# Kernel tuning notes

Hardware: AMD Instinct MI355X
Metric: run time of the kernel (lower is better)

The kernel has to match this reference:

```python
import jax, jax.numpy as jnp
import numpy as np
from jax import lax

_SOBEL_X = jnp.array([[-1., 0., 1.], [-2., 0., 2.], [-1., 0., 1.]], dtype=jnp.float32)
_SOBEL_Y = jnp.array([[1., 2., 1.], [0., 0., 0.], [-1., -2., -1.]], dtype=jnp.float32)


def rgb2ycrcb(x):
    # x: [B,3,H,W] -> [B,3,H,W] (Y, Cr, Cb)
    R, G, B = x[:, 0], x[:, 1], x[:, 2]
    Y = 0.299 * R + 0.587 * G + 0.114 * B
    Cr = (R - Y) * 0.713 + 0.5
    Cb = (B - Y) * 0.564 + 0.5
    return jnp.stack([Y, Cr, Cb], axis=1)


def depthwise_sobel(x):
    # x: [B,3,H,W]; per-channel 3x3 cross-correlation with SAME padding (matches F.conv2d pad=1)
    C = x.shape[1]
    wx = jnp.broadcast_to(_SOBEL_X[None, None], (C, 1, 3, 3))
    wy = jnp.broadcast_to(_SOBEL_Y[None, None], (C, 1, 3, 3))
    dn = ('NCHW', 'OIHW', 'NCHW')
    gx = lax.conv_general_dilated(x, wx, (1, 1), 'SAME', feature_group_count=C, dimension_numbers=dn)
    gy = lax.conv_general_dilated(x, wy, (1, 1), 'SAME', feature_group_count=C, dimension_numbers=dn)
    return gx, gy


def adjust_gamma(img, gamma, gain=1.0):
    # torchvision float path: clamp(gain * img**gamma, 0, 1)
    return jnp.clip(gain * img ** gamma, 0.0, 1.0)


def adjust_contrast(img, factor):
    # torchvision: blend with per-image mean of grayscale, then clamp
    gray = 0.2989 * img[:, 0:1] + 0.587 * img[:, 1:2] + 0.114 * img[:, 2:3]
    mean = jnp.mean(gray, axis=(1, 2, 3), keepdims=True)
    return jnp.clip(factor * img + (1.0 - factor) * mean, 0.0, 1.0)


def l1(a, b):
    return jnp.mean(jnp.abs(a - b))


def fusion_loss(input_vis, input_ir, output, Mask):
    Fuse = output * Mask
    ycc_fuse = rgb2ycrcb(Fuse)
    Cr_F, Cb_F = ycc_fuse[:, 1:2], ycc_fuse[:, 2:3]

    R_vis = adjust_gamma(input_vis, 0.5, 1.0)
    ycc_vis = rgb2ycrcb(R_vis)
    Cr_V, Cb_V = ycc_vis[:, 1:2], ycc_vis[:, 2:3]

    R_ir = adjust_contrast(input_ir, 1.8)

    fgx, fgy = depthwise_sobel(Fuse)
    vgx, vgy = depthwise_sobel(R_vis)
    igx, igy = depthwise_sobel(R_ir)

    joint_gx = jnp.maximum(vgx, igx)
    joint_gy = jnp.maximum(vgy, igy)
    joint_int = jnp.maximum(R_vis, R_ir)

    con_loss = l1(Fuse, joint_int)
    grad_loss = 0.5 * l1(fgx, joint_gx) + 0.5 * l1(fgy, joint_gy)
    color_loss = l1(Cb_F, Cb_V) + l1(Cr_F, Cr_V)
    return 0.5 * con_loss + 0.2 * grad_loss + 1.0 * color_loss


def setup_inputs() -> dict:
    key = jax.random.key(0)
    k1, k2, k3, k4 = jax.random.split(key, 4)
    B, C, H, W = 16, 3, 512, 512
    return {
        'input_vis': jax.random.uniform(k1, (B, C, H, W), dtype=jnp.float32),
        'input_ir': jax.random.uniform(k2, (B, C, H, W), dtype=jnp.float32),
        'output': jax.random.uniform(k3, (B, C, H, W), dtype=jnp.float32),
        'Mask': jax.random.uniform(k4, (B, C, H, W), dtype=jnp.float32),
    }


def reference(input_vis, input_ir, output, Mask):
    return fusion_loss(input_vis, input_ir, output, Mask)
```

## Files before the change

### kernel.cpp

```cpp
#include <hip/hip_runtime.h>
#include <math.h>

#define Bn 16
#define Cn 3
#define Hn 512
#define Wn 512
#define HWn (Hn*Wn)
#define CHWn (Cn*HWn)
#define Rr 4

__device__ __forceinline__ float clamp01(float x) {
    return fminf(fmaxf(x, 0.0f), 1.0f);
}

__global__ __launch_bounds__(256) void gray_mean_kernel(
        const float* __restrict__ ir, float* __restrict__ ws)
{
    const int b = blockIdx.y;
    const int tid = threadIdx.x;
    const float* base = ir + (size_t)b * CHWn;

    float sr = 0.f, sg = 0.f, sb = 0.f;
#pragma unroll
    for (int k = 0; k < 8; ++k) {
        size_t px = (size_t)blockIdx.x * 8192 + (size_t)(k * 256 + tid) * 4;
        float4 r4 = *(const float4*)(base + px);
        float4 g4 = *(const float4*)(base + HWn + px);
        float4 b4 = *(const float4*)(base + 2 * HWn + px);
        sr += (r4.x + r4.y) + (r4.z + r4.w);
        sg += (g4.x + g4.y) + (g4.z + g4.w);
        sb += (b4.x + b4.y) + (b4.z + b4.w);
    }
    float s = 0.2989f * sr + 0.587f * sg + 0.114f * sb;

#pragma unroll
    for (int off = 32; off; off >>= 1) s += __shfl_down(s, off, 64);

    __shared__ float red[4];
    if ((tid & 63) == 0) red[tid >> 6] = s;
    __syncthreads();
    if (tid == 0) atomicAdd(&ws[b], (red[0] + red[1]) + (red[2] + red[3]));
}

__global__ __launch_bounds__(256) void fusion_main_kernel(
        const float* __restrict__ vis, const float* __restrict__ ir,
        const float* __restrict__ outp, const float* __restrict__ mask,
        float* __restrict__ ws)
{
    const int tid = threadIdx.x;
    const int tx = tid & 127;
    const int sy = tid >> 7;
    const int b  = blockIdx.y;
    const int y0 = (blockIdx.x * 2 + sy) * Rr;
    const int x0 = tx * 4;

    const float mean_b = ws[b] * (1.0f / (float)HWn);
    const float moff = 0.8f * mean_b;

    const size_t bb = (size_t)b * CHWn;
    const float* pv = vis  + bb;
    const float* pi = ir   + bb;
    const float* po = outp + bb;
    const float* pm = mask + bb;

    float conA = 0.f, gxA = 0.f, gyA = 0.f;

#define DECL_SLOT(S)                                                          \
    float wf##S##_0, wf##S##_1, wf##S##_2, wf##S##_3, wf##S##_4, wf##S##_5;   \
    float wv##S##_0, wv##S##_1, wv##S##_2, wv##S##_3, wv##S##_4, wv##S##_5;   \
    float wi##S##_0, wi##S##_1, wi##S##_2, wi##S##_3, wi##S##_4, wi##S##_5;

#define LOAD_ROW(Y, S)                                                        \
    do {                                                                      \
        const int y_ = (Y);                                                   \
        if ((unsigned)y_ < (unsigned)Hn) {                                    \
            const size_t o = (size_t)y_ * Wn + x0;                            \
            float4 o4 = *(const float4*)(o_ + o);                             \
            float4 m4 = *(const float4*)(m_ + o);                             \
            float4 v4 = *(const float4*)(v_ + o);                             \
            float4 i4 = *(const float4*)(i_ + o);                             \
            float oL = 0.f, mL = 0.f, vL = 0.f, iL = 0.f;                     \
            float oR = 0.f, mR = 0.f, vR = 0.f, iR = 0.f;                     \
            if (x0 > 0)      { oL = o_[o - 1]; mL = m_[o - 1];                \
                               vL = v_[o - 1]; iL = i_[o - 1]; }              \
            if (x0 + 4 < Wn) { oR = o_[o + 4]; mR = m_[o + 4];                \
                               vR = v_[o + 4]; iR = i_[o + 4]; }              \
            wf##S##_0 = oL * mL;     wf##S##_1 = o4.x * m4.x;                 \
            wf##S##_2 = o4.y * m4.y; wf##S##_3 = o4.z * m4.z;                 \
            wf##S##_4 = o4.w * m4.w; wf##S##_5 = oR * mR;                     \
            wv##S##_0 = clamp01(sqrtf(vL));   wv##S##_1 = clamp01(sqrtf(v4.x)); \
            wv##S##_2 = clamp01(sqrtf(v4.y)); wv##S##_3 = clamp01(sqrtf(v4.z)); \
            wv##S##_4 = clamp01(sqrtf(v4.w)); wv##S##_5 = clamp01(sqrtf(vR));   \
            wi##S##_0 = clamp01(fmaf(1.8f, iL,   -moff));                     \
            wi##S##_1 = clamp01(fmaf(1.8f, i4.x, -moff));                     \
            wi##S##_2 = clamp01(fmaf(1.8f, i4.y, -moff));                     \
            wi##S##_3 = clamp01(fmaf(1.8f, i4.z, -moff));                     \
            wi##S##_4 = clamp01(fmaf(1.8f, i4.w, -moff));                     \
            wi##S##_5 = clamp01(fmaf(1.8f, iR,   -moff));                     \
        } else {                                                              \
            wf##S##_0=0.f; wf##S##_1=0.f; wf##S##_2=0.f;                      \
            wf##S##_3=0.f; wf##S##_4=0.f; wf##S##_5=0.f;                      \
            wv##S##_0=0.f; wv##S##_1=0.f; wv##S##_2=0.f;                      \
            wv##S##_3=0.f; wv##S##_4=0.f; wv##S##_5=0.f;                      \
            wi##S##_0=0.f; wi##S##_1=0.f; wi##S##_2=0.f;                      \
            wi##S##_3=0.f; wi##S##_4=0.f; wi##S##_5=0.f;                      \
        }                                                                     \
    } while (0)

#define SOBEL_J(A, B, C, J0, J1, J2)                                          \
    do {                                                                      \
        float gxf = (wf##A##_##J2 - wf##A##_##J0) + 2.f * (wf##B##_##J2 - wf##B##_##J0) + (wf##C##_##J2 - wf##C##_##J0); \
        float gyf = (wf##A##_##J0 + 2.f * wf##A##_##J1 + wf##A##_##J2) - (wf##C##_##J0 + 2.f * wf##C##_##J1 + wf##C##_##J2); \
        float gxv = (wv##A##_##J2 - wv##A##_##J0) + 2.f * (wv##B##_##J2 - wv##B##_##J0) + (wv##C##_##J2 - wv##C##_##J0); \
        float gyv = (wv##A##_##J0 + 2.f * wv##A##_##J1 + wv##A##_##J2) - (wv##C##_##J0 + 2.f * wv##C##_##J1 + wv##C##_##J2); \
        float gxi = (wi##A##_##J2 - wi##A##_##J0) + 2.f * (wi##B##_##J2 - wi##B##_##J0) + (wi##C##_##J2 - wi##C##_##J0); \
        float gyi = (wi##A##_##J0 + 2.f * wi##A##_##J1 + wi##A##_##J2) - (wi##C##_##J0 + 2.f * wi##C##_##J1 + wi##C##_##J2); \
        gxA  += fabsf(gxf - fmaxf(gxv, gxi));                                 \
        gyA  += fabsf(gyf - fmaxf(gyv, gyi));                                 \
        conA += fabsf(wf##B##_##J1 - fmaxf(wv##B##_##J1, wi##B##_##J1));      \
    } while (0)

#define STEP(A, B, C)                                                         \
    SOBEL_J(A, B, C, 0, 1, 2); SOBEL_J(A, B, C, 1, 2, 3);                     \
    SOBEL_J(A, B, C, 2, 3, 4); SOBEL_J(A, B, C, 3, 4, 5)

    for (int c = 0; c < 3; ++c) {
        const float* v_ = pv + (size_t)c * HWn;
        const float* i_ = pi + (size_t)c * HWn;
        const float* o_ = po + (size_t)c * HWn;
        const float* m_ = pm + (size_t)c * HWn;

        DECL_SLOT(0) DECL_SLOT(1) DECL_SLOT(2)

        LOAD_ROW(y0 - 1, 0);
        LOAD_ROW(y0,     1);
        LOAD_ROW(y0 + 1, 2); STEP(0, 1, 2);
        LOAD_ROW(y0 + 2, 0); STEP(1, 2, 0);
        LOAD_ROW(y0 + 3, 1); STEP(2, 0, 1);
        LOAD_ROW(y0 + 4, 2); STEP(0, 1, 2);
    }
#undef STEP
#undef SOBEL_J
#undef LOAD_ROW
#undef DECL_SLOT

    float crA = 0.f, cbA = 0.f;
    {
        for (int y = y0; y < y0 + Rr; ++y) {
            size_t o = (size_t)y * Wn + x0;
            float4 oR = *(const float4*)(po + o);
            float4 oG = *(const float4*)(po + HWn + o);
            float4 oB = *(const float4*)(po + 2 * HWn + o);
            float4 mR = *(const float4*)(pm + o);
            float4 mG = *(const float4*)(pm + HWn + o);
            float4 mB = *(const float4*)(pm + 2 * HWn + o);
            float4 vR = *(const float4*)(pv + o);
            float4 vG = *(const float4*)(pv + HWn + o);
            float4 vB = *(const float4*)(pv + 2 * HWn + o);
#define COLOR_PX(FR, FG, FB, VR, VG, VB)                                      \
            do {                                                              \
                float fr = (FR), fg = (FG), fb = (FB);                        \
                float vr = (VR), vg = (VG), vb = (VB);                        \
                float fY = 0.299f * fr + 0.587f * fg + 0.114f * fb;           \
                float vY = 0.299f * vr + 0.587f * vg + 0.114f * vb;           \
                crA += fabsf((fr - fY) * 0.713f - (vr - vY) * 0.713f);        \
                cbA += fabsf((fb - fY) * 0.564f - (vb - vY) * 0.564f);        \
            } while (0)
            COLOR_PX(oR.x * mR.x, oG.x * mG.x, oB.x * mB.x,
                     clamp01(sqrtf(vR.x)), clamp01(sqrtf(vG.x)), clamp01(sqrtf(vB.x)));
            COLOR_PX(oR.y * mR.y, oG.y * mG.y, oB.y * mB.y,
                     clamp01(sqrtf(vR.y)), clamp01(sqrtf(vG.y)), clamp01(sqrtf(vB.y)));
            COLOR_PX(oR.z * mR.z, oG.z * mG.z, oB.z * mB.z,
                     clamp01(sqrtf(vR.z)), clamp01(sqrtf(vG.z)), clamp01(sqrtf(vB.z)));
            COLOR_PX(oR.w * mR.w, oG.w * mG.w, oB.w * mB.w,
                     clamp01(sqrtf(vR.w)), clamp01(sqrtf(vG.w)), clamp01(sqrtf(vB.w)));
#undef COLOR_PX
        }
    }

    auto wred = [](float x) {
#pragma unroll
        for (int off = 32; off; off >>= 1) x += __shfl_down(x, off, 64);
        return x;
    };
    conA = wred(conA); gxA = wred(gxA); gyA = wred(gyA);
    crA  = wred(crA);  cbA = wred(cbA);

    __shared__ float red[5][4];
    const int lane = tid & 63, w = tid >> 6;
    if (lane == 0) {
        red[0][w] = conA; red[1][w] = gxA; red[2][w] = gyA;
        red[3][w] = crA;  red[4][w] = cbA;
    }
    __syncthreads();
    if (tid < 5) {
        float s = (red[tid][0] + red[tid][1]) + (red[tid][2] + red[tid][3]);
        atomicAdd(&ws[16 + tid], s);
    }
}

__global__ void finalize_kernel(const float* __restrict__ ws, float* __restrict__ out)
{
    if (threadIdx.x == 0 && blockIdx.x == 0) {
        const float invN3 = 1.0f / (float)((size_t)Bn * Cn * HWn);
        const float invN1 = 1.0f / (float)((size_t)Bn * HWn);
        float con = ws[16] * invN3;
        float gx  = ws[17] * invN3;
        float gy  = ws[18] * invN3;
        float cr  = ws[19] * invN1;
        float cb  = ws[20] * invN1;
        out[0] = 0.5f * con + 0.2f * (0.5f * gx + 0.5f * gy) + (cb + cr);
    }
}

extern "C" void kernel_launch(void* const* d_in, const int* in_sizes, int n_in,
                              void* d_out, int out_size, void* d_ws, size_t ws_size,
                              hipStream_t stream)
{
    const float* vis = (const float*)d_in[0];
    const float* ir  = (const float*)d_in[1];
    const float* out = (const float*)d_in[2];
    const float* msk = (const float*)d_in[3];
    float* ws = (float*)d_ws;

    hipMemsetAsync(ws, 0, 32 * sizeof(float), stream);

    gray_mean_kernel<<<dim3(32, Bn), 256, 0, stream>>>(ir, ws);
    fusion_main_kernel<<<dim3(Hn / (2 * Rr), Bn), 256, 0, stream>>>(vis, ir, out, msk, ws);
    finalize_kernel<<<1, 64, 0, stream>>>(ws, (float*)d_out);
}
```

Baseline: 244.6 us.

## Fuse gray-mean, main loss and finalize into one persistent kernel with grid barrier

Merges the three kernels into one 512-block launch. Each block first computes a partial IR grayscale mean, then all blocks wait at an atomic-counter grid barrier, after which each block processes two batch images' strips. The last block to finish computes the final loss, replacing the separate finalize launch. This removes two kernel launches and their gaps, but needs all 512 blocks co-resident for the spin barrier to avoid deadlock, and halves the main-phase block count (1024 to 512) while doubling the work per block.

```diff
diff --git a/kernel.cpp b/kernel.cpp
--- a/kernel.cpp
+++ b/kernel.cpp
@@ -8,62 +8,12 @@
 #define HWn (Hn*Wn)
 #define CHWn (Cn*HWn)
 #define Rr 4
+#define NBLK 512
 
 __device__ __forceinline__ float clamp01(float x) {
     return fminf(fmaxf(x, 0.0f), 1.0f);
 }
 
-__global__ __launch_bounds__(256) void gray_mean_kernel(
-        const float* __restrict__ ir, float* __restrict__ ws)
-{
-    const int b = blockIdx.y;
-    const int tid = threadIdx.x;
-    const float* base = ir + (size_t)b * CHWn;
-
-    float sr = 0.f, sg = 0.f, sb = 0.f;
-#pragma unroll
-    for (int k = 0; k < 8; ++k) {
-        size_t px = (size_t)blockIdx.x * 8192 + (size_t)(k * 256 + tid) * 4;
-        float4 r4 = *(const float4*)(base + px);
-        float4 g4 = *(const float4*)(base + HWn + px);
-        float4 b4 = *(const float4*)(base + 2 * HWn + px);
-        sr += (r4.x + r4.y) + (r4.z + r4.w);
-        sg += (g4.x + g4.y) + (g4.z + g4.w);
-        sb += (b4.x + b4.y) + (b4.z + b4.w);
-    }
-    float s = 0.2989f * sr + 0.587f * sg + 0.114f * sb;
-
-#pragma unroll
-    for (int off = 32; off; off >>= 1) s += __shfl_down(s, off, 64);
-
-    __shared__ float red[4];
-    if ((tid & 63) == 0) red[tid >> 6] = s;
-    __syncthreads();
-    if (tid == 0) atomicAdd(&ws[b], (red[0] + red[1]) + (red[2] + red[3]));
-}
-
-__global__ __launch_bounds__(256) void fusion_main_kernel(
-        const float* __restrict__ vis, const float* __restrict__ ir,
-        const float* __restrict__ outp, const float* __restrict__ mask,
-        float* __restrict__ ws)
-{
-    const int tid = threadIdx.x;
-    const int tx = tid & 127;
-    const int sy = tid >> 7;
-    const int b  = blockIdx.y;
-    const int y0 = (blockIdx.x * 2 + sy) * Rr;
-    const int x0 = tx * 4;
-
-    const float mean_b = ws[b] * (1.0f / (float)HWn);
-    const float moff = 0.8f * mean_b;
-
-    const size_t bb = (size_t)b * CHWn;
-    const float* pv = vis  + bb;
-    const float* pi = ir   + bb;
-    const float* po = outp + bb;
-    const float* pm = mask + bb;
-
-    float conA = 0.f, gxA = 0.f, gyA = 0.f;
 
 #define DECL_SLOT(S)                                                          \
     float wf##S##_0, wf##S##_1, wf##S##_2, wf##S##_3, wf##S##_4, wf##S##_5;   \
@@ -97,6 +47,8 @@
             wi##S##_3 = clamp01(fmaf(1.8f, i4.z, -moff));                     \
             wi##S##_4 = clamp01(fmaf(1.8f, i4.w, -moff));                     \
             wi##S##_5 = clamp01(fmaf(1.8f, iR,   -moff));                     \
+            if (x0 == 0)      { wf##S##_0 = 0.f; wv##S##_0 = 0.f; wi##S##_0 = 0.f; } \
+            if (x0 + 4 >= Wn) { wf##S##_5 = 0.f; wv##S##_5 = 0.f; wi##S##_5 = 0.f; } \
         } else {                                                              \
             wf##S##_0=0.f; wf##S##_1=0.f; wf##S##_2=0.f;                      \
             wf##S##_3=0.f; wf##S##_4=0.f; wf##S##_5=0.f;                      \
@@ -124,6 +76,12 @@
     SOBEL_J(A, B, C, 0, 1, 2); SOBEL_J(A, B, C, 1, 2, 3);                     \
     SOBEL_J(A, B, C, 2, 3, 4); SOBEL_J(A, B, C, 3, 4, 5)
 
+__device__ __forceinline__ void strip_body(
+        const float* __restrict__ pv, const float* __restrict__ pi,
+        const float* __restrict__ po, const float* __restrict__ pm,
+        int y0, int x0, float moff,
+        float& conA, float& gxA, float& gyA, float& crA, float& cbA)
+{
     for (int c = 0; c < 3; ++c) {
         const float* v_ = pv + (size_t)c * HWn;
         const float* i_ = pi + (size_t)c * HWn;
@@ -139,77 +97,134 @@
         LOAD_ROW(y0 + 3, 1); STEP(2, 0, 1);
         LOAD_ROW(y0 + 4, 2); STEP(0, 1, 2);
     }
-#undef STEP
-#undef SOBEL_J
-#undef LOAD_ROW
-#undef DECL_SLOT
-
-    float crA = 0.f, cbA = 0.f;
+
+    for (int y = y0; y < y0 + Rr; ++y) {
+        size_t o = (size_t)y * Wn + x0;
+        float4 oR = *(const float4*)(po + o);
+        float4 oG = *(const float4*)(po + HWn + o);
+        float4 oB = *(const float4*)(po + 2 * HWn + o);
+        float4 mR = *(const float4*)(pm + o);
+        float4 mG = *(const float4*)(pm + HWn + o);
+        float4 mB = *(const float4*)(pm + 2 * HWn + o);
+        float4 vR = *(const float4*)(pv + o);
+        float4 vG = *(const float4*)(pv + HWn + o);
+        float4 vB = *(const float4*)(pv + 2 * HWn + o);
+#define COLOR_PX(FR, FG, FB, VR, VG, VB)                                      \
+        do {                                                                  \
+            float fr = (FR), fg = (FG), fb = (FB);                            \
+            float vr = (VR), vg = (VG), vb = (VB);                            \
+            float fY = 0.299f * fr + 0.587f * fg + 0.114f * fb;               \
+            float vY = 0.299f * vr + 0.587f * vg + 0.114f * vb;               \
+            crA += fabsf((fr - fY) * 0.713f - (vr - vY) * 0.713f);            \
+            cbA += fabsf((fb - fY) * 0.564f - (vb - vY) * 0.564f);            \
+        } while (0)
+        COLOR_PX(oR.x * mR.x, oG.x * mG.x, oB.x * mB.x,
+                 clamp01(sqrtf(vR.x)), clamp01(sqrtf(vG.x)), clamp01(sqrtf(vB.x)));
+        COLOR_PX(oR.y * mR.y, oG.y * mG.y, oB.y * mB.y,
+                 clamp01(sqrtf(vR.y)), clamp01(sqrtf(vG.y)), clamp01(sqrtf(vB.y)));
+        COLOR_PX(oR.z * mR.z, oG.z * mG.z, oB.z * mB.z,
+                 clamp01(sqrtf(vR.z)), clamp01(sqrtf(vG.z)), clamp01(sqrtf(vB.z)));
+        COLOR_PX(oR.w * mR.w, oG.w * mG.w, oB.w * mB.w,
+                 clamp01(sqrtf(vR.w)), clamp01(sqrtf(vG.w)), clamp01(sqrtf(vB.w)));
+#undef COLOR_PX
+    }
+}
+
+__global__ __launch_bounds__(256, 4) void fused_kernel(
+        const float* __restrict__ vis, const float* __restrict__ ir,
+        const float* __restrict__ outp, const float* __restrict__ mask,
+        float* __restrict__ ws, float* __restrict__ out)
+{
+    __shared__ float red[5][4];
+    const int bid = blockIdx.x;
+    const int tid = threadIdx.x;
+    int* wsi = (int*)ws;
+
     {
-        for (int y = y0; y < y0 + Rr; ++y) {
-            size_t o = (size_t)y * Wn + x0;
-            float4 oR = *(const float4*)(po + o);
-            float4 oG = *(const float4*)(po + HWn + o);
-            float4 oB = *(const float4*)(po + 2 * HWn + o);
-            float4 mR = *(const float4*)(pm + o);
-            float4 mG = *(const float4*)(pm + HWn + o);
-            float4 mB = *(const float4*)(pm + 2 * HWn + o);
-            float4 vR = *(const float4*)(pv + o);
-            float4 vG = *(const float4*)(pv + HWn + o);
-            float4 vB = *(const float4*)(pv + 2 * HWn + o);
-#define COLOR_PX(FR, FG, FB, VR, VG, VB)                                      \
-            do {                                                              \
-                float fr = (FR), fg = (FG), fb = (FB);                        \
-                float vr = (VR), vg = (VG), vb = (VB);                        \
-                float fY = 0.299f * fr + 0.587f * fg + 0.114f * fb;           \
-                float vY = 0.299f * vr + 0.587f * vg + 0.114f * vb;           \
-                crA += fabsf((fr - fY) * 0.713f - (vr - vY) * 0.713f);        \
-                cbA += fabsf((fb - fY) * 0.564f - (vb - vY) * 0.564f);        \
-            } while (0)
-            COLOR_PX(oR.x * mR.x, oG.x * mG.x, oB.x * mB.x,
-                     clamp01(sqrtf(vR.x)), clamp01(sqrtf(vG.x)), clamp01(sqrtf(vB.x)));
-            COLOR_PX(oR.y * mR.y, oG.y * mG.y, oB.y * mB.y,
-                     clamp01(sqrtf(vR.y)), clamp01(sqrtf(vG.y)), clamp01(sqrtf(vB.y)));
-            COLOR_PX(oR.z * mR.z, oG.z * mG.z, oB.z * mB.z,
-                     clamp01(sqrtf(vR.z)), clamp01(sqrtf(vG.z)), clamp01(sqrtf(vB.z)));
-            COLOR_PX(oR.w * mR.w, oG.w * mG.w, oB.w * mB.w,
-                     clamp01(sqrtf(vR.w)), clamp01(sqrtf(vG.w)), clamp01(sqrtf(vB.w)));
-#undef COLOR_PX
+        const int gb = bid >> 5;
+        const int gx = bid & 31;
+        const float* base = ir + (size_t)gb * CHWn;
+        float sr = 0.f, sg = 0.f, sb = 0.f;
+#pragma unroll
+        for (int k = 0; k < 8; ++k) {
+            size_t px = (size_t)gx * 8192 + (size_t)(k * 256 + tid) * 4;
+            float4 r4 = *(const float4*)(base + px);
+            float4 g4 = *(const float4*)(base + HWn + px);
+            float4 b4 = *(const float4*)(base + 2 * HWn + px);
+            sr += (r4.x + r4.y) + (r4.z + r4.w);
+            sg += (g4.x + g4.y) + (g4.z + g4.w);
+            sb += (b4.x + b4.y) + (b4.z + b4.w);
         }
-    }
-
-    auto wred = [](float x) {
-#pragma unroll
-        for (int off = 32; off; off >>= 1) x += __shfl_down(x, off, 64);
-        return x;
+        float s = 0.2989f * sr + 0.587f * sg + 0.114f * sb;
+#pragma unroll
+        for (int off = 32; off; off >>= 1) s += __shfl_down(s, off, 64);
+        if ((tid & 63) == 0) red[0][tid >> 6] = s;
+        __syncthreads();
+        if (tid == 0) {
+            atomicAdd(&ws[gb], (red[0][0] + red[0][1]) + (red[0][2] + red[0][3]));
+            __threadfence();
+            atomicAdd(&wsi[24], 1);
+            while (__hip_atomic_load(&wsi[24], __ATOMIC_RELAXED,
+                                     __HIP_MEMORY_SCOPE_AGENT) < NBLK)
+                __builtin_amdgcn_s_sleep(8);
+        }
+        __syncthreads();
+    }
+
+    const int x  = bid & 63;
+    const int b1 = bid >> 6;
+    const float mean1 = __hip_atomic_load(&ws[b1],     __ATOMIC_RELAXED,
+                                          __HIP_MEMORY_SCOPE_AGENT) * (1.0f / (float)HWn);
+    const float mean2 = __hip_atomic_load(&ws[b1 + 8], __ATOMIC_RELAXED,
+                                          __HIP_MEMORY_SCOPE_AGENT) * (1.0f / (float)HWn);
+
+    const int tx = tid & 127;
+    const int sy = tid >> 7;
+    const int y0 = (x * 2 + sy) * Rr;
+    const int x0 = tx * 4;
+
+    float conA = 0.f, gxA = 0.f, gyA = 0.f, crA = 0.f, cbA = 0.f;
+
+#pragma unroll 1
+    for (int jj = 0; jj < 2; ++jj) {
+        const int bb_idx = b1 + jj * 8;
+        const float moff = 0.8f * (jj ? mean2 : mean1);
+        const size_t bb = (size_t)bb_idx * CHWn;
+        strip_body(vis + bb, ir + bb, outp + bb, mask + bb,
+                   y0, x0, moff, conA, gxA, gyA, crA, cbA);
+    }
+
+    auto wred = [](float v) {
+#pragma unroll
+        for (int off = 32; off; off >>= 1) v += __shfl_down(v, off, 64);
+        return v;
     };
     conA = wred(conA); gxA = wred(gxA); gyA = wred(gyA);
     crA  = wred(crA);  cbA = wred(cbA);
 
-    __shared__ float red[5][4];
     const int lane = tid & 63, w = tid >> 6;
+    __syncthreads();
     if (lane == 0) {
         red[0][w] = conA; red[1][w] = gxA; red[2][w] = gyA;
         red[3][w] = crA;  red[4][w] = cbA;
     }
     __syncthreads();
-    if (tid < 5) {
-        float s = (red[tid][0] + red[tid][1]) + (red[tid][2] + red[tid][3]);
-        atomicAdd(&ws[16 + tid], s);
-    }
-}
-
-__global__ void finalize_kernel(const float* __restrict__ ws, float* __restrict__ out)
-{
-    if (threadIdx.x == 0 && blockIdx.x == 0) {
-        const float invN3 = 1.0f / (float)((size_t)Bn * Cn * HWn);
-        const float invN1 = 1.0f / (float)((size_t)Bn * HWn);
-        float con = ws[16] * invN3;
-        float gx  = ws[17] * invN3;
-        float gy  = ws[18] * invN3;
-        float cr  = ws[19] * invN1;
-        float cb  = ws[20] * invN1;
-        out[0] = 0.5f * con + 0.2f * (0.5f * gx + 0.5f * gy) + (cb + cr);
+    if (tid == 0) {
+#pragma unroll
+        for (int r = 0; r < 5; ++r)
+            atomicAdd(&ws[16 + r], (red[r][0] + red[r][1]) + (red[r][2] + red[r][3]));
+        __threadfence();
+        int old = atomicAdd(&wsi[25], 1);
+        if (old == NBLK - 1) {
+            const float invN3 = 1.0f / (float)((size_t)Bn * Cn * HWn);
+            const float invN1 = 1.0f / (float)((size_t)Bn * HWn);
+            float con = __hip_atomic_load(&ws[16], __ATOMIC_RELAXED, __HIP_MEMORY_SCOPE_AGENT) * invN3;
+            float gx  = __hip_atomic_load(&ws[17], __ATOMIC_RELAXED, __HIP_MEMORY_SCOPE_AGENT) * invN3;
+            float gy  = __hip_atomic_load(&ws[18], __ATOMIC_RELAXED, __HIP_MEMORY_SCOPE_AGENT) * invN3;
+            float cr  = __hip_atomic_load(&ws[19], __ATOMIC_RELAXED, __HIP_MEMORY_SCOPE_AGENT) * invN1;
+            float cb  = __hip_atomic_load(&ws[20], __ATOMIC_RELAXED, __HIP_MEMORY_SCOPE_AGENT) * invN1;
+            out[0] = 0.5f * con + 0.2f * (0.5f * gx + 0.5f * gy) + (cb + cr);
+        }
     }
 }
 
@@ -224,8 +239,5 @@
     float* ws = (float*)d_ws;
 
     hipMemsetAsync(ws, 0, 32 * sizeof(float), stream);
-
-    gray_mean_kernel<<<dim3(32, Bn), 256, 0, stream>>>(ir, ws);
-    fusion_main_kernel<<<dim3(Hn / (2 * Rr), Bn), 256, 0, stream>>>(vis, ir, out, msk, ws);
-    finalize_kernel<<<1, 64, 0, stream>>>(ws, (float*)d_out);
-}
+    fused_kernel<<<dim3(NBLK), 256, 0, stream>>>(vis, ir, out, msk, ws, (float*)d_out);
+}
```

Result: slower. 400.5 us (+63.7%).
